# Kernel tuning notes

Hardware: AMD Instinct MI355X
Metric: run time of the kernel (lower is better)

The kernel has to match this reference:

```python
import jax, jax.numpy as jnp
import numpy as np

N, K, H = 20000, 32, 128
DIN = 3 * H   # num_hidden + num_in = 128 + 256
FF = 4 * H
SCALE = 30.0
EPS = 1e-5


def setup_inputs() -> dict:
    key = jax.random.key(0)
    ks = jax.random.split(key, 32)
    s = 0.05
    w = lambda k, shp: jax.random.normal(k, shp, dtype=jnp.float32) * s
    return {
        "h_V": jax.random.normal(ks[0], (N, H), dtype=jnp.float32),
        "h_E": jax.random.normal(ks[1], (N, K, H), dtype=jnp.float32),
        "mask_V": jnp.ones((N,), dtype=jnp.float32),
        "mask_attend": jnp.ones((N, K), dtype=jnp.float32),
        # message MLP 1 (weights stored [in, out])
        "W1_w": w(ks[2], (DIN, H)), "W1_b": jnp.zeros((H,)),
        "W2_w": w(ks[3], (H, H)),   "W2_b": jnp.zeros((H,)),
        "W3_w": w(ks[4], (H, H)),   "W3_b": jnp.zeros((H,)),
        # message MLP 2
        "W11_w": w(ks[5], (DIN, H)), "W11_b": jnp.zeros((H,)),
        "W12_w": w(ks[6], (H, H)),   "W12_b": jnp.zeros((H,)),
        "W13_w": w(ks[7], (H, H)),   "W13_b": jnp.zeros((H,)),
        # position-wise FFN
        "Win_w": w(ks[8], (H, FF)),  "Win_b": jnp.zeros((FF,)),
        "Wout_w": w(ks[9], (FF, H)), "Wout_b": jnp.zeros((H,)),
        # LayerNorms
        "ln1_g": jnp.ones((H,)), "ln1_b": jnp.zeros((H,)),
        "ln2_g": jnp.ones((H,)), "ln2_b": jnp.zeros((H,)),
        "ln3_g": jnp.ones((H,)), "ln3_b": jnp.zeros((H,)),
        "E_idx": jax.random.randint(ks[10], (N, K), 0, N),
    }


def _ln(x, g, b):
    m = jnp.mean(x, -1, keepdims=True)
    v = jnp.mean(jnp.square(x - m), -1, keepdims=True)
    return (x - m) * jax.lax.rsqrt(v + EPS) * g + b


def _gelu(x):
    return jax.nn.gelu(x, approximate=False)  # torch default (erf) GELU


def reference(h_V, h_E, mask_V, mask_attend,
              W1_w, W1_b, W2_w, W2_b, W3_w, W3_b,
              W11_w, W11_b, W12_w, W12_b, W13_w, W13_b,
              Win_w, Win_b, Wout_w, Wout_b,
              ln1_g, ln1_b, ln2_g, ln2_b, ln3_g, ln3_b,
              E_idx):
    n, k = E_idx.shape

    def edge_feats(hv):
        nbr = hv[E_idx]  # [N,K,H] gather of neighbor node features
        hv_exp = jnp.broadcast_to(hv[:, None, :], (n, k, hv.shape[-1]))
        return jnp.concatenate([hv_exp, h_E, nbr], -1)  # [N,K,3H]

    # --- node update ---
    h_EV = edge_feats(h_V)
    msg = _gelu(h_EV @ W1_w + W1_b)
    msg = _gelu(msg @ W2_w + W2_b)
    msg = msg @ W3_w + W3_b
    msg = mask_attend[..., None] * msg
    dh = jnp.sum(msg, axis=-2) / SCALE
    hV = _ln(h_V + dh, ln1_g, ln1_b)
    dh = _gelu(hV @ Win_w + Win_b) @ Wout_w + Wout_b
    hV = _ln(hV + dh, ln2_g, ln2_b)
    hV = mask_V[:, None] * hV

    # --- edge update ---
    h_EV = edge_feats(hV)
    msg = _gelu(h_EV @ W11_w + W11_b)
    msg = _gelu(msg @ W12_w + W12_b)
    msg = msg @ W13_w + W13_b
    hE = _ln(h_E + msg, ln3_g, ln3_b)
    return (hV, hE)
```

## Files before the change

### kernel.cpp

```cpp
#include <hip/hip_runtime.h>
#include <hip/hip_bf16.h>
#include <cstdint>
#include <cstddef>

#define NN 20000
#define KK 32
#define HH 128
#define FFD 512
#define LN_EPS 1e-5f

typedef __attribute__((ext_vector_type(8))) short bf16x8;
typedef __attribute__((ext_vector_type(4))) float f32x4;

__device__ __forceinline__ short f2b(float f){
  __hip_bfloat16 h = __float2bfloat16(f);
  return __builtin_bit_cast(short, h);
}
__device__ __forceinline__ float b2f(short s){
  union { unsigned int u; float f; } v; v.u = ((unsigned int)(unsigned short)s) << 16; return v.f;
}
__device__ __forceinline__ unsigned int pk2(float a, float b){
  return (unsigned int)(unsigned short)f2b(a) | ((unsigned int)(unsigned short)f2b(b) << 16);
}
__device__ __forceinline__ float gelu_fast(float x){
  float u = x * __builtin_fmaf(0.10294278f, x*x, 2.3022082f);
  float e = __builtin_amdgcn_exp2f(u);
  float r = __builtin_amdgcn_rcpf(1.0f + e);
  return __builtin_fmaf(-x, r, x);
}
__device__ __forceinline__ f32x4 MFMA(bf16x8 a, bf16x8 b, f32x4 c){
  return __builtin_amdgcn_mfma_f32_16x16x32_bf16(a, b, c, 0, 0, 0);
}

__global__ __launch_bounds__(256) void enc_pack(
    const float* __restrict__ W1, const float* __restrict__ W2, const float* __restrict__ W3,
    const float* __restrict__ W11, const float* __restrict__ W12, const float* __restrict__ W13,
    const float* __restrict__ Win, const float* __restrict__ Wout,
    short* __restrict__ pk)
{
  const int stride = gridDim.x * blockDim.x;
  for (int idx = blockIdx.x*blockDim.x + threadIdx.x; idx < 294912; idx += stride){
    const float* src = W2; int srow = 0, k, n, NT, NCOLS, base;
    if (idx < 163840){
      int slot = idx >> 14, e = idx & 16383;
      k = e >> 7; n = e & 127; NT = 8; NCOLS = 128; base = slot << 14;
      switch (slot){
        case 0: src = W1;  srow = 0;   break;
        case 1: src = W1;  srow = 256; break;
        case 2: src = W1;  srow = 128; break;
        case 3: src = W2;  srow = 0;   break;
        case 4: src = W3;  srow = 0;   break;
        case 5: src = W11; srow = 0;   break;
        case 6: src = W11; srow = 256; break;
        case 7: src = W11; srow = 128; break;
        case 8: src = W12; srow = 0;   break;
        default: src = W13; srow = 0;  break;
      }
    } else if (idx < 229376){
      int e = idx - 163840; k = e >> 9; n = e & 511; NT = 32; NCOLS = 512; src = Win; base = 163840;
    } else {
      int e = idx - 229376; k = e >> 7; n = e & 127; NT = 8; NCOLS = 128; src = Wout; base = 229376;
    }
    float v = src[(srow + k)*NCOLS + n];
    int out = base + (((k>>5)*NT + (n>>4))*64 + ((k>>3)&3)*16 + (n&15))*8 + (k&7);
    pk[out] = f2b(v);
  }
}

__global__ __launch_bounds__(256, 2) void enc_proj(
    const float* __restrict__ X, const short* __restrict__ pkU, const short* __restrict__ pkZ,
    const float* __restrict__ biasU, short* __restrict__ U, short* __restrict__ Z)
{
  const int lane = threadIdx.x & 63, w = threadIdx.x >> 6;
  const int kgrp = lane >> 4, ccol = lane & 15;
  const int row0 = blockIdx.x*64 + w*16;
  const int arow = row0 + (lane & 15);
  f32x4 accU[8], accZ[8];
  #pragma unroll
  for (int nf=0;nf<8;nf++){ accU[nf] = (f32x4){0,0,0,0}; accZ[nf] = (f32x4){0,0,0,0}; }
  #pragma unroll
  for (int kt=0;kt<4;kt++){
    bf16x8 af = {0,0,0,0,0,0,0,0};
    if (arow < NN){
      const float4* p = (const float4*)(X + (size_t)arow*HH + kt*32 + kgrp*8);
      float4 v0 = p[0], v1 = p[1];
      af[0]=f2b(v0.x); af[1]=f2b(v0.y); af[2]=f2b(v0.z); af[3]=f2b(v0.w);
      af[4]=f2b(v1.x); af[5]=f2b(v1.y); af[6]=f2b(v1.z); af[7]=f2b(v1.w);
    }
    #pragma unroll
    for (int nf=0;nf<8;nf++){
      bf16x8 bu = *(const bf16x8*)(pkU + (((kt<<3)+nf)*64 + lane)*8);
      accU[nf] = MFMA(af, bu, accU[nf]);
      bf16x8 bz = *(const bf16x8*)(pkZ + (((kt<<3)+nf)*64 + lane)*8);
      accZ[nf] = MFMA(af, bz, accZ[nf]);
    }
  }
  #pragma unroll
  for (int nf=0;nf<8;nf++){
    #pragma unroll
    for (int r=0;r<4;r++){
      int grow = row0 + kgrp*4 + r;
      if (grow < NN){
        int col = nf*16 + ccol;
        U[(size_t)grow*HH + col] = f2b(accU[nf][r] + biasU[col]);
        Z[(size_t)grow*HH + col] = f2b(accZ[nf][r]);
      }
    }
  }
}

#define LSTR 136
template<int PASS, int EM>
__global__ __launch_bounds__(512, 4) void enc_mlp3(
    const float* __restrict__ hE,
    const short* __restrict__ Ub, const short* __restrict__ Zb,
    const int*  __restrict__ Eidx,
    const float* __restrict__ maskAtt,
    const float* __restrict__ hV,
    const float* __restrict__ lnG, const float* __restrict__ lnB,
    const short* __restrict__ pkL1,
    const short* __restrict__ pkL2, const float* __restrict__ bias2,
    const short* __restrict__ pkL3, const float* __restrict__ bias3,
    float* __restrict__ outP,
    short* __restrict__ hEs)
{
  __shared__ __align__(16) short sBuf[128*LSTR];
  __shared__ __align__(16) short sW[16384];
  __shared__ float sB23[256];
  __shared__ float sPart[8][128];

  const int i0 = blockIdx.x*4;
  const int t = threadIdx.x;
  const int lane = t & 63, w = t >> 6;
  const int kgrp = lane >> 4, ccol = lane & 15;
  const int node = i0 + (w >> 1);
  const int rw = w*16;
  const size_t ebase = (size_t)i0*KK;

  if (t < 256) sB23[t] = (t < 128) ? bias2[t] : bias3[t-128];

  #pragma unroll
  for (int it=0; it<4; it++){
    int idx = it*512 + t;
    *(int4*)(sW + idx*8) = *(const int4*)(pkL1 + idx*8);
  }

  if constexpr (EM == 1 && PASS == 1){
    const short* srcS = hEs + (ebase + rw)*HH;
    #pragma unroll
    for (int it=0; it<4; it++){
      int r16 = it*4 + (lane>>4);
      int c16 = lane & 15;
      int4 v = *(const int4*)(srcS + (size_t)r16*HH + c16*8);
      *(int4*)(sBuf + (rw + r16)*LSTR + c16*8) = v;
    }
  } else {
    const float4* src = (const float4*)(hE + (ebase + rw)*HH);
    #pragma unroll
    for (int it=0; it<8; it++){
      int r = it*2 + (lane>>5);
      int c4 = lane & 31;
      float4 v = src[r*32 + c4];
      uint2 p; p.x = pk2(v.x, v.y); p.y = pk2(v.z, v.w);
      *(uint2*)(sBuf + (rw + r)*LSTR + c4*4) = p;
      if constexpr (EM == 1 && PASS == 0)
        *(uint2*)(hEs + (ebase + rw + r)*HH + c4*4) = p;
    }
  }
  __syncthreads();

  const short* sRow = sBuf + (rw + ccol)*LSTR;
  f32x4 acc[8];

  #pragma unroll
  for (int nf=0;nf<8;nf++) acc[nf] = (f32x4){0,0,0,0};
  #pragma unroll
  for (int kt=0;kt<4;kt++){
    bf16x8 af = *(const bf16x8*)(sRow + kt*32 + kgrp*8);
    #pragma unroll
    for (int nf=0;nf<8;nf++){
      bf16x8 b = *(const bf16x8*)(sW + (((kt<<3)+nf)*64 + lane)*8);
      acc[nf] = MFMA(af, b, acc[nf]);
    }
  }
  {
    const int zrow = rw + (lane >> 2);
    const int seg0 = lane & 3;
    const int jj = Eidx[i0*KK + zrow];
    const int4* zsrc = (const int4*)(Zb + (size_t)jj*HH);
    int4 z0 = zsrc[seg0];
    int4 z1 = zsrc[seg0 + 4];
    int4 z2 = zsrc[seg0 + 8];
    int4 z3 = zsrc[seg0 + 12];
    *(int4*)(sBuf + zrow*LSTR + (seg0     )*8) = z0;
    *(int4*)(sBuf + zrow*LSTR + (seg0 + 4 )*8) = z1;
    *(int4*)(sBuf + zrow*LSTR + (seg0 + 8 )*8) = z2;
    *(int4*)(sBuf + zrow*LSTR + (seg0 + 12)*8) = z3;
  }
  __syncthreads();
  #pragma unroll
  for (int it=0; it<4; it++){
    int idx = it*512 + t;
    *(int4*)(sW + idx*8) = *(const int4*)(pkL2 + idx*8);
  }
  #pragma unroll
  for (int nf=0;nf<8;nf++){
    float uv = b2f(Ub[(size_t)node*HH + nf*16 + ccol]);
    #pragma unroll
    for (int r=0;r<4;r++){
      short* p = sBuf + (rw + kgrp*4 + r)*LSTR + nf*16 + ccol;
      float v = acc[nf][r] + uv + b2f(*p);
      *p = f2b(gelu_fast(v));
    }
  }
  __syncthreads();

  #pragma unroll
  for (int nf=0;nf<8;nf++) acc[nf] = (f32x4){0,0,0,0};
  #pragma unroll
  for (int kt=0;kt<4;kt++){
    bf16x8 af = *(const bf16x8*)(sRow + kt*32 + kgrp*8);
    #pragma unroll
    for (int nf=0;nf<8;nf++){
      bf16x8 b = *(const bf16x8*)(sW + (((kt<<3)+nf)*64 + lane)*8);
      acc[nf] = MFMA(af, b, acc[nf]);
    }
  }
  __syncthreads();
  #pragma unroll
  for (int it=0; it<4; it++){
    int idx = it*512 + t;
    *(int4*)(sW + idx*8) = *(const int4*)(pkL3 + idx*8);
  }
  #pragma unroll
  for (int nf=0;nf<8;nf++){
    float b2v = sB23[nf*16 + ccol];
    #pragma unroll
    for (int r=0;r<4;r++){
      short* p = sBuf + (rw + kgrp*4 + r)*LSTR + nf*16 + ccol;
      *p = f2b(gelu_fast(acc[nf][r] + b2v));
    }
  }
  __syncthreads();

  #pragma unroll
  for (int nf=0;nf<8;nf++) acc[nf] = (f32x4){0,0,0,0};
  #pragma unroll
  for (int kt=0;kt<4;kt++){
    bf16x8 af = *(const bf16x8*)(sRow + kt*32 + kgrp*8);
    #pragma unroll
    for (int nf=0;nf<8;nf++){
      bf16x8 b = *(const bf16x8*)(sW + (((kt<<3)+nf)*64 + lane)*8);
      acc[nf] = MFMA(af, b, acc[nf]);
    }
  }

  if (PASS == 0){
    float m[4];
    {
      const float4 mv = *(const float4*)(maskAtt + ebase + rw + kgrp*4);
      m[0]=mv.x; m[1]=mv.y; m[2]=mv.z; m[3]=mv.w;
    }
    #pragma unroll
    for (int nf=0;nf<8;nf++){
      float b3v = sB23[128 + nf*16 + ccol];
      float s = 0.f;
      #pragma unroll
      for (int r=0;r<4;r++) s = __builtin_fmaf(acc[nf][r] + b3v, m[r], s);
      s += __shfl_xor(s, 16);
      s += __shfl_xor(s, 32);
      if (kgrp == 0) sPart[w][nf*16 + ccol] = s;
    }
    __syncthreads();
    if ((w & 1) == 0){
      float c0 = sPart[w][lane]    + sPart[w+1][lane];
      float c1 = sPart[w][64+lane] + sPart[w+1][64+lane];
      float x0 = hV[(size_t)node*HH + lane]      + c0*(1.0f/30.0f);
      float x1 = hV[(size_t)node*HH + 64 + lane] + c1*(1.0f/30.0f);
      float sm = x0 + x1, sq = x0*x0 + x1*x1;
      #pragma unroll
      for (int off=1; off<64; off<<=1){
        sm += __shfl_xor(sm, off);
        sq += __shfl_xor(sq, off);
      }
      float mean = sm*(1.f/128.f);
      float var  = sq*(1.f/128.f) - mean*mean;
      float inv  = rsqrtf(var + LN_EPS);
      outP[(size_t)node*HH + lane]      = (x0-mean)*inv*lnG[lane]    + lnB[lane];
      outP[(size_t)node*HH + 64 + lane] = (x1-mean)*inv*lnG[64+lane] + lnB[64+lane];
    }
  } else {
    float rs[4] = {0,0,0,0}, rq[4] = {0,0,0,0};
    #pragma unroll
    for (int nf=0;nf<8;nf++){
      float b3v = sB23[128 + nf*16 + ccol];
      #pragma unroll
      for (int r=0;r<4;r++){
        int row = rw + kgrp*4 + r, col = nf*16 + ccol;
        float hres;
        if constexpr (EM == 1) hres = b2f(hEs[(ebase + row)*HH + col]);
        else                   hres = hE[(ebase + row)*HH + col];
        float x = acc[nf][r] + b3v + hres;
        acc[nf][r] = x;
        rs[r] += x; rq[r] += x*x;
      }
    }
    #pragma unroll
    for (int off=1; off<16; off<<=1){
      #pragma unroll
      for (int r=0;r<4;r++){
        rs[r] += __shfl_xor(rs[r], off);
        rq[r] += __shfl_xor(rq[r], off);
      }
    }
    #pragma unroll
    for (int r=0;r<4;r++){
      float mean = rs[r]*(1.f/128.f);
      float var  = rq[r]*(1.f/128.f) - mean*mean;
      float inv  = rsqrtf(var + LN_EPS);
      #pragma unroll
      for (int nf=0;nf<8;nf++){
        int row = rw + kgrp*4 + r, col = nf*16 + ccol;
        __builtin_nontemporal_store((acc[nf][r]-mean)*inv*lnG[col] + lnB[col],
                                    &outP[(ebase + row)*HH + col]);
      }
    }
  }
}

__global__ __launch_bounds__(256, 2) void enc_ffn(
    const float* __restrict__ X,
    const short* __restrict__ pkWin, const float* __restrict__ bin,
    const short* __restrict__ pkWout, const float* __restrict__ bout,
    const float* __restrict__ g2, const float* __restrict__ b2ln,
    const float* __restrict__ maskV,
    float* __restrict__ out)
{
  __shared__ short sT[64*512];
  const int t = threadIdx.x, lane = t & 63, w = t >> 6;
  const int kgrp = lane >> 4, ccol = lane & 15;
  const int row0 = blockIdx.x*64;
  const int arow = row0 + w*16 + (lane & 15);
  f32x4 acc[32];
  #pragma unroll
  for (int nf=0;nf<32;nf++) acc[nf] = (f32x4){0,0,0,0};
  #pragma unroll
  for (int kt=0;kt<4;kt++){
    bf16x8 af = {0,0,0,0,0,0,0,0};
    if (arow < NN){
      const float4* p = (const float4*)(X + (size_t)arow*HH + kt*32 + kgrp*8);
      float4 v0 = p[0], v1 = p[1];
      af[0]=f2b(v0.x); af[1]=f2b(v0.y); af[2]=f2b(v0.z); af[3]=f2b(v0.w);
      af[4]=f2b(v1.x); af[5]=f2b(v1.y); af[6]=f2b(v1.z); af[7]=f2b(v1.w);
    }
    #pragma unroll
    for (int nf=0;nf<32;nf++){
      bf16x8 b = *(const bf16x8*)(pkWin + ((size_t)((kt<<5)+nf)*64 + lane)*8);
      acc[nf] = MFMA(af, b, acc[nf]);
    }
  }
  #pragma unroll
  for (int nf=0;nf<32;nf++){
    #pragma unroll
    for (int r=0;r<4;r++){
      int rl = w*16 + kgrp*4 + r, col = nf*16 + ccol;
      sT[rl*512 + (col ^ ((rl&7)<<3))] = f2b(gelu_fast(acc[nf][r] + bin[col]));
    }
  }
  f32x4 a2[8];
  #pragma unroll
  for (int nf=0;nf<8;nf++) a2[nf] = (f32x4){0,0,0,0};
  const int rl_a = w*16 + (lane & 15);
  #pragma unroll
  for (int kt=0;kt<16;kt++){
    int base = kt*32 + kgrp*8;
    bf16x8 af = *(const bf16x8*)(sT + rl_a*512 + (base ^ ((rl_a&7)<<3)));
    #pragma unroll
    for (int nf=0;nf<8;nf++){
      bf16x8 b = *(const bf16x8*)(pkWout + (((kt<<3)+nf)*64 + lane)*8);
      a2[nf] = MFMA(af, b, a2[nf]);
    }
  }
  float rsum[4] = {0,0,0,0}, rsq[4] = {0,0,0,0};
  #pragma unroll
  for (int nf=0;nf<8;nf++){
    #pragma unroll
    for (int r=0;r<4;r++){
      int grow = row0 + w*16 + kgrp*4 + r, col = nf*16 + ccol;
      float prev = (grow < NN) ? X[(size_t)grow*HH + col] : 0.f;
      float x = a2[nf][r] + bout[col] + prev;
      a2[nf][r] = x;
      rsum[r] += x; rsq[r] += x*x;
    }
  }
  #pragma unroll
  for (int off=1; off<16; off<<=1){
    #pragma unroll
    for (int r=0;r<4;r++){
      rsum[r] += __shfl_xor(rsum[r], off);
      rsq[r]  += __shfl_xor(rsq[r], off);
    }
  }
  #pragma unroll
  for (int r=0;r<4;r++){
    int grow = row0 + w*16 + kgrp*4 + r;
    float mean = rsum[r]*(1.f/128.f);
    float var  = rsq[r]*(1.f/128.f) - mean*mean;
    float inv  = rsqrtf(var + LN_EPS);
    float mv   = (grow < NN) ? maskV[grow] : 0.f;
    #pragma unroll
    for (int nf=0;nf<8;nf++){
      int col = nf*16 + ccol;
      if (grow < NN)
        out[(size_t)grow*HH + col] = mv * ((a2[nf][r]-mean)*inv*g2[col] + b2ln[col]);
    }
  }
}

extern "C" void kernel_launch(void* const* d_in, const int* in_sizes, int n_in,
                              void* d_out, int out_size, void* d_ws, size_t ws_size,
                              hipStream_t stream)
{
  const float* h_V   = (const float*)d_in[0];
  const float* h_E   = (const float*)d_in[1];
  const float* maskV = (const float*)d_in[2];
  const float* maskA = (const float*)d_in[3];
  const float* W1w  = (const float*)d_in[4];  const float* W1b  = (const float*)d_in[5];
  const float* W2w  = (const float*)d_in[6];  const float* W2b  = (const float*)d_in[7];
  const float* W3w  = (const float*)d_in[8];  const float* W3b  = (const float*)d_in[9];
  const float* W11w = (const float*)d_in[10]; const float* W11b = (const float*)d_in[11];
  const float* W12w = (const float*)d_in[12]; const float* W12b = (const float*)d_in[13];
  const float* W13w = (const float*)d_in[14]; const float* W13b = (const float*)d_in[15];
  const float* Winw = (const float*)d_in[16]; const float* Winb = (const float*)d_in[17];
  const float* Woutw= (const float*)d_in[18]; const float* Woutb= (const float*)d_in[19];
  const float* ln1g = (const float*)d_in[20]; const float* ln1b = (const float*)d_in[21];
  const float* ln2g = (const float*)d_in[22]; const float* ln2b = (const float*)d_in[23];
  const float* ln3g = (const float*)d_in[24]; const float* ln3b = (const float*)d_in[25];
  const int*   Eidx = (const int*)d_in[26];

  float* outV = (float*)d_out;
  float* outE = outV + (size_t)NN*HH;

  char* ws = (char*)d_ws;
  short* pk = (short*)ws;
  const short* pkW1a  = pk + 0*16384;
  const short* pkW1c  = pk + 1*16384;
  const short* pkW1bb = pk + 2*16384;
  const short* pkW2   = pk + 3*16384;
  const short* pkW3   = pk + 4*16384;
  const short* pkW11a = pk + 5*16384;
  const short* pkW11c = pk + 6*16384;
  const short* pkW11bb= pk + 7*16384;
  const short* pkW12  = pk + 8*16384;
  const short* pkW13  = pk + 9*16384;
  const short* pkWin  = pk + 163840;
  const short* pkWout = pk + 229376;

  short* U1 = (short*)(ws + 1048576);
  short* Z1 = (short*)(ws + 6291456);
  short* U2 = (short*)(ws + 11534336);
  short* Z2 = (short*)(ws + 16777216);
  float* hVmid = (float*)(ws + 22020096);
  short* hEs = (short*)(ws + 33554432);

  const bool em = ws_size >= (size_t)33554432 + (size_t)NN*KK*HH*2;

  enc_pack<<<288, 256, 0, stream>>>(W1w, W2w, W3w, W11w, W12w, W13w, Winw, Woutw, pk);
  enc_proj<<<313, 256, 0, stream>>>(h_V, pkW1a, pkW1c, W1b, U1, Z1);
  if (em){
    enc_mlp3<0,1><<<NN/4, 512, 0, stream>>>(h_E, U1, Z1, Eidx, maskA, h_V,
                                            ln1g, ln1b, pkW1bb, pkW2, W2b, pkW3, W3b, hVmid, hEs);
  } else {
    enc_mlp3<0,0><<<NN/4, 512, 0, stream>>>(h_E, U1, Z1, Eidx, maskA, h_V,
                                            ln1g, ln1b, pkW1bb, pkW2, W2b, pkW3, W3b, hVmid, nullptr);
  }
  enc_ffn<<<313, 256, 0, stream>>>(hVmid, pkWin, Winb, pkWout, Woutb,
                                   ln2g, ln2b, maskV, outV);
  enc_proj<<<313, 256, 0, stream>>>(outV, pkW11a, pkW11c, W11b, U2, Z2);
  if (em){
    enc_mlp3<1,1><<<NN/4, 512, 0, stream>>>(h_E, U2, Z2, Eidx, nullptr, nullptr,
                                            ln3g, ln3b, pkW11bb, pkW12, W12b, pkW13, W13b, outE, hEs);
  } else {
    enc_mlp3<1,0><<<NN/4, 512, 0, stream>>>(h_E, U2, Z2, Eidx, nullptr, nullptr,
                                            ln3g, ln3b, pkW11bb, pkW12, W12b, pkW13, W13b, outE, nullptr);
  }
}
```

Baseline: 417.2 us.

## Load packed weights directly to LDS and fold node bias into accumulator init

Replaces the register-staged weight copies into shared memory with global_load_lds direct-to-LDS transfers of 16 bytes per lane. The per-node U vector is preloaded into registers and used to seed the MFMA accumulators instead of being added in the epilogue. The bf16 copy of h_E is written with nontemporal stores. This is meant to cut VGPR traffic and load latency on the weight swaps, but correctness depends on the LDS-direct loads completing before the barrier.

```diff
diff --git a/kernel.cpp b/kernel.cpp
--- a/kernel.cpp
+++ b/kernel.cpp
@@ -30,6 +30,12 @@
 }
 __device__ __forceinline__ f32x4 MFMA(bf16x8 a, bf16x8 b, f32x4 c){
   return __builtin_amdgcn_mfma_f32_16x16x32_bf16(a, b, c, 0, 0, 0);
+}
+__device__ __forceinline__ void gload_lds16(const short* g, short* l){
+  __builtin_amdgcn_global_load_lds(
+      (const __attribute__((address_space(1))) void*)g,
+      (__attribute__((address_space(3))) void*)l,
+      16, 0, 0);
 }
 
 __global__ __launch_bounds__(256) void enc_pack(
@@ -139,11 +145,13 @@
 
   if (t < 256) sB23[t] = (t < 128) ? bias2[t] : bias3[t-128];
 
-  #pragma unroll
-  for (int it=0; it<4; it++){
-    int idx = it*512 + t;
-    *(int4*)(sW + idx*8) = *(const int4*)(pkL1 + idx*8);
-  }
+  float ureg[8];
+  #pragma unroll
+  for (int nf=0; nf<8; nf++) ureg[nf] = b2f(Ub[(size_t)node*HH + nf*16 + ccol]);
+
+  #pragma unroll
+  for (int i=0;i<4;i++)
+    gload_lds16(pkL1 + (w*4 + i)*512 + lane*8, sW + (w*4 + i)*512);
 
   if constexpr (EM == 1 && PASS == 1){
     const short* srcS = hEs + (ebase + rw)*HH;
@@ -161,10 +169,12 @@
       int r = it*2 + (lane>>5);
       int c4 = lane & 31;
       float4 v = src[r*32 + c4];
-      uint2 p; p.x = pk2(v.x, v.y); p.y = pk2(v.z, v.w);
-      *(uint2*)(sBuf + (rw + r)*LSTR + c4*4) = p;
+      unsigned long long p = (unsigned long long)pk2(v.x, v.y)
+                           | ((unsigned long long)pk2(v.z, v.w) << 32);
+      *(unsigned long long*)(sBuf + (rw + r)*LSTR + c4*4) = p;
       if constexpr (EM == 1 && PASS == 0)
-        *(uint2*)(hEs + (ebase + rw + r)*HH + c4*4) = p;
+        __builtin_nontemporal_store(p,
+            (unsigned long long*)(hEs + (ebase + rw + r)*HH + c4*4));
     }
   }
   __syncthreads();
@@ -173,7 +183,7 @@
   f32x4 acc[8];
 
   #pragma unroll
-  for (int nf=0;nf<8;nf++) acc[nf] = (f32x4){0,0,0,0};
+  for (int nf=0;nf<8;nf++) acc[nf] = (f32x4){ureg[nf],ureg[nf],ureg[nf],ureg[nf]};
   #pragma unroll
   for (int kt=0;kt<4;kt++){
     bf16x8 af = *(const bf16x8*)(sRow + kt*32 + kgrp*8);
@@ -199,17 +209,14 @@
   }
   __syncthreads();
   #pragma unroll
-  for (int it=0; it<4; it++){
-    int idx = it*512 + t;
-    *(int4*)(sW + idx*8) = *(const int4*)(pkL2 + idx*8);
-  }
+  for (int i=0;i<4;i++)
+    gload_lds16(pkL2 + (w*4 + i)*512 + lane*8, sW + (w*4 + i)*512);
   #pragma unroll
   for (int nf=0;nf<8;nf++){
-    float uv = b2f(Ub[(size_t)node*HH + nf*16 + ccol]);
     #pragma unroll
     for (int r=0;r<4;r++){
       short* p = sBuf + (rw + kgrp*4 + r)*LSTR + nf*16 + ccol;
-      float v = acc[nf][r] + uv + b2f(*p);
+      float v = acc[nf][r] + b2f(*p);
       *p = f2b(gelu_fast(v));
     }
   }
@@ -228,10 +235,8 @@
   }
   __syncthreads();
   #pragma unroll
-  for (int it=0; it<4; it++){
-    int idx = it*512 + t;
-    *(int4*)(sW + idx*8) = *(const int4*)(pkL3 + idx*8);
-  }
+  for (int i=0;i<4;i++)
+    gload_lds16(pkL3 + (w*4 + i)*512 + lane*8, sW + (w*4 + i)*512);
   #pragma unroll
   for (int nf=0;nf<8;nf++){
     float b2v = sB23[nf*16 + ccol];
```

Result: no change. 411.0 us (-1.5%).
